# Optimization experiments

Hardware: AMD Instinct MI355X
Metric: run time of the kernel (lower is better)

Reference implementation:

```python
import jax, jax.numpy as jnp
from jax import lax
import numpy as np

TAU = 10.0      # tauSr == tauRef
THR = 1.0       # theta
WIDTH = 1.0     # tauRho (surrogate width)
SCALE = 1.0     # scaleRho (surrogate scale)
DECAY = float(np.exp(-1.0 / TAU))


@jax.custom_vjp
def _heaviside(v):
    # spike = 1[v >= theta]
    return (v >= THR).astype(v.dtype)

def _heaviside_fwd(v):
    return _heaviside(v), v

def _heaviside_bwd(v, g):
    # SLAYER exponential surrogate pdf: scaleRho/tauRho * exp(-|v-theta|/tauRho)
    return (g * (SCALE / WIDTH) * jnp.exp(-jnp.abs(v - THR) / WIDTH),)

_heaviside.defvjp(_heaviside_fwd, _heaviside_bwd)


def _conv2d(x, w, pad):
    # x: (B, Cin, H, W), w: (Cout, Cin, kh, kw); SLAYER convs have no bias
    return lax.conv_general_dilated(
        x, w, window_strides=(1, 1), padding=[(pad, pad), (pad, pad)],
        dimension_numbers=("NCHW", "OIHW", "NCHW"))


def _sumpool(x, k):
    # SLAYER pool = sum over kxk window (times a learned scalar applied outside)
    B, C, H, W = x.shape
    return x.reshape(B, C, H // k, k, W // k, k).sum(axis=(3, 5))


def _psp(seq):
    # exponential synaptic (PSP) filter along time: s[t] = a*s[t-1] + x[t]
    a = jnp.asarray(DECAY, seq.dtype)
    def step(s, x_t):
        s = a * s + x_t
        return s, s
    _, out = lax.scan(step, jnp.zeros_like(seq[0]), seq)
    return out  # (T, ...)


def _spikes(u):
    # thresholded spiking with decaying refractory feedback (scaleRef=1):
    # v[t] = u[t] - r[t]; s[t] = 1[v >= theta]; r[t+1] = b*(r[t] + theta*s[t])
    b = jnp.asarray(DECAY, u.dtype)
    def step(r, u_t):
        s = _heaviside(u_t - r)
        r_next = b * (r + THR * s)
        return r_next, s
    _, out = lax.scan(step, jnp.zeros_like(u[0]), u)
    return out  # (T, ...)


def _forward(x, conv1_w, conv2_w, lin_w, w_pool1, w_pool2):
    N, T, C, H, W = x.shape  # (64, 100, 2, 32, 32)
    h = _conv2d(x.reshape(N * T, C, H, W), conv1_w, 2)        # (NT, 4, 32, 32)
    h = _sumpool(h, 4) * w_pool1                               # (NT, 4, 8, 8)
    h = h.reshape(N, T, 4, 8, 8).swapaxes(0, 1)                # (T, N, 4, 8, 8)
    s1 = _spikes(_psp(h))                                      # (T, N, 4, 8, 8)
    h2 = _conv2d(s1.reshape(T * N, 4, 8, 8), conv2_w, 1)       # (TN, 8, 8, 8)
    h2 = (_sumpool(h2, 2) * w_pool2).reshape(T, N, 8, 4, 4)    # (T, N, 8, 4, 4)
    s2 = _spikes(_psp(h2))                                     # (T, N, 8, 4, 4)
    # dense = full-spatial conv (2, 8, 4, 4) -> (N, T, 2)
    return jnp.einsum("tnchw,ochw->nto", s2, lin_w)


def setup_inputs() -> dict:
    key = jax.random.key(0)
    ks = jax.random.split(key, 4)
    x = (jax.random.uniform(ks[0], (64, 100, 2, 32, 32)) < 0.1).astype(jnp.float32)
    conv1_w = jax.random.normal(ks[1], (4, 2, 5, 5), jnp.float32) * 0.3
    conv2_w = jax.random.normal(ks[2], (8, 4, 3, 3), jnp.float32) * 0.3
    lin_w = jax.random.normal(ks[3], (2, 8, 4, 4), jnp.float32) * 0.3
    w_pool1 = jnp.float32(1.0 / 16.0)  # 1.1*theta / (16 * 1.1)
    w_pool2 = jnp.float32(1.0 / 4.0)   # 1.1*theta / (4 * 1.1)
    return {"x": x, "conv1_w": conv1_w, "conv2_w": conv2_w, "lin_w": lin_w,
            "w_pool1": w_pool1, "w_pool2": w_pool2}


def reference(x, conv1_w, conv2_w, lin_w, w_pool1, w_pool2):
    return _forward(x, conv1_w, conv2_w, lin_w, w_pool1, w_pool2)
```

## Files before the change

kernel.cpp:

```cpp
#include <hip/hip_runtime.h>


#define DECAY 0.9048374180359595f

#define BAR_LGKM() asm volatile("s_waitcnt lgkmcnt(0)\n\ts_barrier" ::: "memory")
#define FENCE_LGKM() asm volatile("s_waitcnt lgkmcnt(0)" ::: "memory")

typedef __attribute__((ext_vector_type(8))) _Float16 half8;

__global__ __launch_bounds__(64) void k1(const float* __restrict__ x,
        const float* __restrict__ w1, const float* __restrict__ wp1,
        float* __restrict__ u1, float* __restrict__ out) {
    __shared__ __align__(16) float xs[2 * 1296];
    __shared__ __align__(16) float wl[512];
    __shared__ __align__(16) float w1s[200];
    const int lane = threadIdx.x;
    const int frame = blockIdx.x;
    const int n = frame / 100, t = frame % 100;

    if (frame < 50) {
        #pragma unroll
        for (int q = 0; q < 4; ++q)
            out[frame * 256 + q * 64 + lane] = 0.f;
    }

    #pragma unroll
    for (int q = 0; q < 4; ++q) {
        const int m = q * 64 + lane;
        if (m < 200) w1s[m] = w1[m];
    }
    FENCE_LGKM();

    {
        const float p1 = wp1[0];
        #pragma unroll
        for (int rep = 0; rep < 8; ++rep) {
            const int idx = rep * 64 + lane;
            const int f = idx & 7, c = (idx >> 3) & 3, e = (idx >> 5) & 7, cin = idx >> 8;
            const int cc = c * 2 + cin;
            int alo = e - 3; if (alo < 0) alo = 0;
            int ahi = e;     if (ahi > 4) ahi = 4;
            int blo = f - 3; if (blo < 0) blo = 0;
            int bhi = f;     if (bhi > 4) bhi = 4;
            float s = 0.f;
            for (int aa = alo; aa <= ahi; ++aa)
                for (int bb = blo; bb <= bhi; ++bb)
                    s += w1s[cc * 25 + aa * 5 + bb];
            wl[(cin * 8 + e) * 32 + c * 8 + f] = s * p1;
        }
    }
    FENCE_LGKM();

    #pragma unroll
    for (int m0 = 0; m0 < 128; m0 += 64) {
        const int m = m0 + lane;
        if (m < 72) {
            const int cin = m / 36, rem = m % 36;
            const int rr = rem / 9, q4 = rem % 9;
            const int pr = (rr == 0) ? 0 : (rr == 1) ? 9 : (rr == 2) ? 26 : 35;
            *(float4*)(xs + cin * 1296 + pr * 36 + q4 * 4) = make_float4(0.f, 0.f, 0.f, 0.f);
        }
    }
    #pragma unroll
    for (int m0 = 0; m0 < 192; m0 += 64) {
        const int m = m0 + lane;
        if (m < 144) {
            const int cin = m / 72, rem = m % 72;
            const int side = rem & 1, pr = rem >> 1;
            *(float2*)(xs + cin * 1296 + pr * 36 + side * 34) = make_float2(0.f, 0.f);
        }
    }
    const float4* xg = (const float4*)(x + (size_t)frame * 2048);
    #pragma unroll
    for (int q = 0; q < 8; ++q) {
        const int m = q * 64 + lane;
        const float4 v = xg[m];
        const int li = 4 * m;
        const int cin = li >> 10, row = (li >> 5) & 31, col = li & 31;
        const int r = row + 2;
        const int pr = (r & 3) * 9 + (r >> 2);
        float* d = xs + cin * 1296 + pr * 36 + col + 2;
        *(float2*)(d)     = make_float2(v.x, v.y);
        *(float2*)(d + 2) = make_float2(v.z, v.w);
    }
    FENCE_LGKM();

    const int cp = lane >> 5;
    const int i  = (lane >> 2) & 7;
    const int jh = (lane >> 1) & 1;
    const int eh = lane & 1;

    float acc[2][4] = {{0.f, 0.f, 0.f, 0.f}, {0.f, 0.f, 0.f, 0.f}};
    const float* tb = xs + (i + eh) * 36 + jh * 16;
    #pragma unroll
    for (int cin = 0; cin < 2; ++cin) {
        #pragma unroll
        for (int et = 0; et < 4; ++et) {
            const int ro = cin * 1296 + et * 9 * 36;
            float xr[20];
            #pragma unroll
            for (int b = 0; b < 5; ++b)
                *(float4*)(xr + 4 * b) = *(const float4*)(tb + ro + 4 * b);
            float wv[16];
            const float* wp = wl + (cin * 8 + eh * 4 + et) * 32 + cp * 16;
            #pragma unroll
            for (int q = 0; q < 4; ++q)
                *(float4*)(wv + 4 * q) = *(const float4*)(wp + 4 * q);
            #pragma unroll
            for (int cl = 0; cl < 2; ++cl) {
                #pragma unroll
                for (int jj = 0; jj < 4; ++jj) {
                    const int o = 4 * jj;
                    acc[cl][jj] += xr[o]*wv[cl*8]     + xr[o+1]*wv[cl*8+1]
                                 + xr[o+2]*wv[cl*8+2] + xr[o+3]*wv[cl*8+3]
                                 + xr[o+4]*wv[cl*8+4] + xr[o+5]*wv[cl*8+5]
                                 + xr[o+6]*wv[cl*8+6] + xr[o+7]*wv[cl*8+7];
                }
            }
        }
    }
    #pragma unroll
    for (int cl = 0; cl < 2; ++cl)
        #pragma unroll
        for (int jj = 0; jj < 4; ++jj)
            acc[cl][jj] += __shfl_xor(acc[cl][jj], 1);

    const float o0 = eh ? acc[1][0] : acc[0][0];
    const float o1 = eh ? acc[1][1] : acc[0][1];
    const float o2 = eh ? acc[1][2] : acc[0][2];
    const float o3 = eh ? acc[1][3] : acc[0][3];
    *(float4*)(u1 + (size_t)n * 25600 + t * 256 + (2 * cp + eh) * 64 + i * 8 + jh * 4) =
        make_float4(o0, o1, o2, o3);
}

__global__ __launch_bounds__(256, 2) void kf(const float* __restrict__ u1,
        const float* __restrict__ w2, const float* __restrict__ wp2,
        const float* __restrict__ lw, float* __restrict__ out) {
    __shared__ __align__(16) _Float16 ls1h[100 * 264];
    __shared__ __align__(16) float    ls2[100 * 20];
    const int tid = threadIdx.x;
    const int bid = blockIdx.x;
    const int n   = (bid & 7) * 8 + (bid >> 6);
    const int oct = (bid >> 3) & 7;
    const int wave = tid >> 6;
    const float a = DECAY;

    if (tid < 64) {
        const float p2 = wp2[0];
        const int cin = tid >> 4, e = (tid >> 2) & 3, f = tid & 3;
        int alo = e - 1; if (alo < 0) alo = 0;
        int ahi = e;     if (ahi > 2) ahi = 2;
        int blo = f - 1; if (blo < 0) blo = 0;
        int bhi = f;     if (bhi > 2) bhi = 2;
        float s = 0.f;
        for (int aa = alo; aa <= ahi; ++aa)
            for (int bb = blo; bb <= bhi; ++bb)
                s += w2[((oct * 4 + cin) * 3 + aa) * 3 + bb];
        ls2[cin * 16 + e * 4 + f] = s * p2;
    }
    __syncthreads();

    float4 wreg[16];
    #pragma unroll
    for (int q = 0; q < 16; ++q)
        wreg[q] = *(const float4*)(ls2 + (q >> 2) * 16 + (q & 3) * 4);

    const float* up = u1 + (size_t)n * 25600 + tid;

    const int sub = tid >> 3, l8 = tid & 7;
    const int i2 = l8 >> 1, jhp = l8 & 1;

    float vbuf[100];
    #pragma unroll
    for (int k = 0; k < 100; ++k) vbuf[k] = up[k * 256];
    {
        float psp = 0.f, rr = 0.f;
        #pragma unroll
        for (int k = 0; k < 100; ++k) {
            psp = a * psp + vbuf[k];
            const float vv = psp - rr;
            const float s = (vv >= 1.f) ? 1.f : 0.f;
            rr = a * (rr + s);
            ls1h[k * 264 + tid] = (_Float16)s;
        }
    }
    BAR_LGKM();

    #pragma unroll 1
    for (int pass = 0; pass < 4; ++pass) {
        const int slot = sub + 32 * pass;
        if (slot < 100) {
            const _Float16* sb = ls1h + slot * 264;
            float acc0 = 0.f, acc1 = 0.f;
            #pragma unroll
            for (int cin = 0; cin < 4; ++cin) {
                #pragma unroll
                for (int e = 0; e < 4; ++e) {
                    const int ri = 2 * i2 + e - 1;
                    const int rc = (ri < 0) ? 0 : (ri > 7 ? 7 : ri);
                    const bool rok = (ri >= 0) && (ri <= 7);
                    const half8 hv = *(const half8*)(sb + cin * 64 + rc * 8);
                    float rr8[8];
                    #pragma unroll
                    for (int m = 0; m < 8; ++m) rr8[m] = (float)hv[m];
                    float xr[6];
                    xr[0] = jhp ? rr8[3] : 0.0f;
                    xr[1] = jhp ? rr8[4] : rr8[0];
                    xr[2] = jhp ? rr8[5] : rr8[1];
                    xr[3] = jhp ? rr8[6] : rr8[2];
                    xr[4] = jhp ? rr8[7] : rr8[3];
                    xr[5] = jhp ? 0.0f   : rr8[4];
                    if (!rok) {
                        #pragma unroll
                        for (int m = 0; m < 6; ++m) xr[m] = 0.0f;
                    }
                    const float4 wf = wreg[cin * 4 + e];
                    acc0 += xr[0] * wf.x; acc0 += xr[1] * wf.y;
                    acc0 += xr[2] * wf.z; acc0 += xr[3] * wf.w;
                    acc1 += xr[2] * wf.x; acc1 += xr[3] * wf.y;
                    acc1 += xr[4] * wf.z; acc1 += xr[5] * wf.w;
                }
            }
            *(float2*)(ls2 + slot * 20 + i2 * 4 + 2 * jhp) =
                make_float2(acc0, acc1);
        }
    }
    BAR_LGKM();

    if (wave == 0 && (tid & 63) < 16) {
        const int cell = tid & 63;
        float ub[100];
        #pragma unroll
        for (int k = 0; k < 100; ++k) ub[k] = ls2[k * 20 + cell];
        float psp2 = 0.f, rr2 = 0.f;
        #pragma unroll
        for (int k = 0; k < 100; ++k) {
            psp2 = a * psp2 + ub[k];
            const float vv = psp2 - rr2;
            const float s = (vv >= 1.f) ? 1.f : 0.f;
            rr2 = a * (rr2 + s);
            ls2[k * 20 + cell] = s;
        }
    }
    BAR_LGKM();

    if (tid < 200) {
        const int t = tid >> 1, o = tid & 1;
        const float* srow = ls2 + t * 20;
        const float* wrow = lw + o * 128 + oct * 16;
        const float4 s0 = *(const float4*)(srow);
        const float4 s1 = *(const float4*)(srow + 4);
        const float4 s2 = *(const float4*)(srow + 8);
        const float4 s3 = *(const float4*)(srow + 12);
        const float4 w0 = *(const float4*)(wrow);
        const float4 w1v = *(const float4*)(wrow + 4);
        const float4 w2v = *(const float4*)(wrow + 8);
        const float4 w3 = *(const float4*)(wrow + 12);
        float v = 0.f;
        v += s0.x * w0.x;  v += s0.y * w0.y;  v += s0.z * w0.z;  v += s0.w * w0.w;
        v += s1.x * w1v.x; v += s1.y * w1v.y; v += s1.z * w1v.z; v += s1.w * w1v.w;
        v += s2.x * w2v.x; v += s2.y * w2v.y; v += s2.z * w2v.z; v += s2.w * w2v.w;
        v += s3.x * w3.x;  v += s3.y * w3.y;  v += s3.z * w3.z;  v += s3.w * w3.w;
        atomicAdd(&out[n * 200 + t * 2 + o], v);
    }
}

extern "C" void kernel_launch(void* const* d_in, const int* in_sizes, int n_in,
                              void* d_out, int out_size, void* d_ws, size_t ws_size,
                              hipStream_t stream) {
    const float* x   = (const float*)d_in[0];
    const float* w1  = (const float*)d_in[1];
    const float* w2  = (const float*)d_in[2];
    const float* lw  = (const float*)d_in[3];
    const float* wp1 = (const float*)d_in[4];
    const float* wp2 = (const float*)d_in[5];

    float* u1  = (float*)d_ws;
    float* out = (float*)d_out;

    k1<<<6400, 64, 0, stream>>>(x, w1, wp1, u1, out);
    kf<<<512, 256, 0, stream>>>(u1, w2, wp2, lw, out);
}
```

Measured before the change: 129.3 us.

## Precompute folded conv1 weights once and split layer-1 spike scan into own kernel

```diff
diff --git a/kernel.cpp b/kernel.cpp
--- a/kernel.cpp
+++ b/kernel.cpp
@@ -8,12 +8,28 @@
 
 typedef __attribute__((ext_vector_type(8))) _Float16 half8;
 
+__global__ __launch_bounds__(128) void k0_fold(const float* __restrict__ w1,
+        const float* __restrict__ wp1, float* __restrict__ wl1) {
+    const int idx = blockIdx.x * 128 + threadIdx.x;
+    const float p1 = wp1[0];
+    const int f = idx & 7, c = (idx >> 3) & 3, e = (idx >> 5) & 7, cin = idx >> 8;
+    const int cc = c * 2 + cin;
+    int alo = e - 3; if (alo < 0) alo = 0;
+    int ahi = e;     if (ahi > 4) ahi = 4;
+    int blo = f - 3; if (blo < 0) blo = 0;
+    int bhi = f;     if (bhi > 4) bhi = 4;
+    float s = 0.f;
+    for (int a = alo; a <= ahi; ++a)
+        for (int b = blo; b <= bhi; ++b)
+            s += w1[cc * 25 + a * 5 + b];
+    wl1[(cin * 8 + e) * 32 + c * 8 + f] = s * p1;
+}
+
 __global__ __launch_bounds__(64) void k1(const float* __restrict__ x,
-        const float* __restrict__ w1, const float* __restrict__ wp1,
-        float* __restrict__ u1, float* __restrict__ out) {
+        const float* __restrict__ wg, float* __restrict__ u1,
+        float* __restrict__ out) {
     __shared__ __align__(16) float xs[2 * 1296];
     __shared__ __align__(16) float wl[512];
-    __shared__ __align__(16) float w1s[200];
     const int lane = threadIdx.x;
     const int frame = blockIdx.x;
     const int n = frame / 100, t = frame % 100;
@@ -24,32 +40,8 @@
             out[frame * 256 + q * 64 + lane] = 0.f;
     }
 
-    #pragma unroll
-    for (int q = 0; q < 4; ++q) {
-        const int m = q * 64 + lane;
-        if (m < 200) w1s[m] = w1[m];
-    }
-    FENCE_LGKM();
-
-    {
-        const float p1 = wp1[0];
-        #pragma unroll
-        for (int rep = 0; rep < 8; ++rep) {
-            const int idx = rep * 64 + lane;
-            const int f = idx & 7, c = (idx >> 3) & 3, e = (idx >> 5) & 7, cin = idx >> 8;
-            const int cc = c * 2 + cin;
-            int alo = e - 3; if (alo < 0) alo = 0;
-            int ahi = e;     if (ahi > 4) ahi = 4;
-            int blo = f - 3; if (blo < 0) blo = 0;
-            int bhi = f;     if (bhi > 4) bhi = 4;
-            float s = 0.f;
-            for (int aa = alo; aa <= ahi; ++aa)
-                for (int bb = blo; bb <= bhi; ++bb)
-                    s += w1s[cc * 25 + aa * 5 + bb];
-            wl[(cin * 8 + e) * 32 + c * 8 + f] = s * p1;
-        }
-    }
-    FENCE_LGKM();
+    *(float4*)(wl + 4 * lane)       = *(const float4*)(wg + 4 * lane);
+    *(float4*)(wl + 256 + 4 * lane) = *(const float4*)(wg + 256 + 4 * lane);
 
     #pragma unroll
     for (int m0 = 0; m0 < 128; m0 += 64) {
@@ -133,17 +125,47 @@
         make_float4(o0, o1, o2, o3);
 }
 
-__global__ __launch_bounds__(256, 2) void kf(const float* __restrict__ u1,
+__global__ __launch_bounds__(256) void k_s(const float* __restrict__ u1,
+        _Float16* __restrict__ s1g) {
+    const int n = blockIdx.x, tid = threadIdx.x;
+    const float a = DECAY;
+    const float* up = u1 + (size_t)n * 25600 + tid;
+    _Float16* sp = s1g + (size_t)n * 26400 + tid;
+
+    float v[100];
+    #pragma unroll
+    for (int k = 0; k < 100; ++k) v[k] = up[k * 256];
+
+    float psp = 0.f, rr = 0.f;
+    #pragma unroll
+    for (int k = 0; k < 100; ++k) {
+        psp = a * psp + v[k];
+        const float vv = psp - rr;
+        const float s = (vv >= 1.f) ? 1.f : 0.f;
+        rr = a * (rr + s);
+        sp[k * 264] = (_Float16)s;
+    }
+}
+
+__global__ __launch_bounds__(256, 2) void kf(const _Float16* __restrict__ s1g,
         const float* __restrict__ w2, const float* __restrict__ wp2,
         const float* __restrict__ lw, float* __restrict__ out) {
     __shared__ __align__(16) _Float16 ls1h[100 * 264];
-    __shared__ __align__(16) float    ls2[100 * 20];
+    __shared__ __align__(16) float    ls2[100 * 20 + 64];
     const int tid = threadIdx.x;
     const int bid = blockIdx.x;
     const int n   = (bid & 7) * 8 + (bid >> 6);
     const int oct = (bid >> 3) & 7;
     const int wave = tid >> 6;
     const float a = DECAY;
+
+    const float4* gs = (const float4*)(s1g + (size_t)n * 26400);
+    float4 st[13];
+    #pragma unroll
+    for (int j = 0; j < 13; ++j) {
+        const int idx = j * 256 + tid;
+        if (idx < 3300) st[j] = gs[idx];
+    }
 
     if (tid < 64) {
         const float p2 = wp2[0];
@@ -156,35 +178,23 @@
         for (int aa = alo; aa <= ahi; ++aa)
             for (int bb = blo; bb <= bhi; ++bb)
                 s += w2[((oct * 4 + cin) * 3 + aa) * 3 + bb];
-        ls2[cin * 16 + e * 4 + f] = s * p2;
-    }
-    __syncthreads();
+        ls2[2000 + cin * 16 + e * 4 + f] = s * p2;
+    }
+
+    #pragma unroll
+    for (int j = 0; j < 13; ++j) {
+        const int idx = j * 256 + tid;
+        if (idx < 3300) *(float4*)((char*)ls1h + idx * 16) = st[j];
+    }
+    BAR_LGKM();
 
     float4 wreg[16];
     #pragma unroll
     for (int q = 0; q < 16; ++q)
-        wreg[q] = *(const float4*)(ls2 + (q >> 2) * 16 + (q & 3) * 4);
-
-    const float* up = u1 + (size_t)n * 25600 + tid;
+        wreg[q] = *(const float4*)(ls2 + 2000 + (q >> 2) * 16 + (q & 3) * 4);
 
     const int sub = tid >> 3, l8 = tid & 7;
     const int i2 = l8 >> 1, jhp = l8 & 1;
-
-    float vbuf[100];
-    #pragma unroll
-    for (int k = 0; k < 100; ++k) vbuf[k] = up[k * 256];
-    {
-        float psp = 0.f, rr = 0.f;
-        #pragma unroll
-        for (int k = 0; k < 100; ++k) {
-            psp = a * psp + vbuf[k];
-            const float vv = psp - rr;
-            const float s = (vv >= 1.f) ? 1.f : 0.f;
-            rr = a * (rr + s);
-            ls1h[k * 264 + tid] = (_Float16)s;
-        }
-    }
-    BAR_LGKM();
 
     #pragma unroll 1
     for (int pass = 0; pass < 4; ++pass) {
@@ -275,9 +285,13 @@
     const float* wp1 = (const float*)d_in[4];
     const float* wp2 = (const float*)d_in[5];
 
-    float* u1  = (float*)d_ws;
-    float* out = (float*)d_out;
-
-    k1<<<6400, 64, 0, stream>>>(x, w1, wp1, u1, out);
-    kf<<<512, 256, 0, stream>>>(u1, w2, wp2, lw, out);
-}
+    float*     u1  = (float*)d_ws;
+    float*     wl1 = u1 + 1638400;
+    _Float16*  s1g = (_Float16*)(wl1 + 512);
+    float*     out = (float*)d_out;
+
+    k0_fold<<<4, 128, 0, stream>>>(w1, wp1, wl1);
+    k1<<<6400, 64, 0, stream>>>(x, wl1, u1, out);
+    k_s<<<64, 256, 0, stream>>>(u1, s1g);
+    kf<<<512, 256, 0, stream>>>(s1g, w2, wp2, lw, out);
+}
```

Result: no change. 126.9 us (-1.8%).
